# Kernel tuning notes

Hardware: AMD Instinct MI355X
Metric: run time of the kernel (lower is better)

The kernel has to match this reference:

```python
import jax, jax.numpy as jnp
import numpy as np

HEIGHT, WIDTH = 480, 640
IN_CHANNEL, OUT_CHANNEL, FILTER = 6, 32, 3
B, N = 8, 16384
X_COL, Y_COL, P_COL = 1, 2, 3


def setup_inputs() -> dict:
    key = jax.random.key(0)
    k1, k2, k3, k4 = jax.random.split(key, 4)
    xytp = jax.random.uniform(k1, (B, N, 4), dtype=jnp.float32)
    features = jax.random.normal(k2, (B, N, IN_CHANNEL), dtype=jnp.float32)
    fan_in = FILTER * FILTER * (IN_CHANNEL + 2)
    W = jax.random.normal(k3, (FILTER, FILTER, IN_CHANNEL + 2, OUT_CHANNEL), dtype=jnp.float32) / jnp.sqrt(jnp.float32(fan_in))
    bias = jax.random.normal(k4, (OUT_CHANNEL,), dtype=jnp.float32) * 0.05
    return {"xytp": xytp, "features": features, "W": W, "bias": bias}


def reference(xytp, features, W, bias):
    Bc, Nc = xytp.shape[:2]
    # polarity channels: [pos, neg] concatenated with extra features -> Cin = in_channel + 2
    p = xytp[..., P_COL:P_COL + 1]
    feat = jnp.concatenate([p, 1.0 - p, features], axis=-1)  # [B, N, Cin]
    # event2image: round normalized coords to integer pixel grid (values in [0, H] / [0, W])
    yy = jnp.round(xytp[..., Y_COL] * HEIGHT).astype(jnp.int32)  # [B, N]
    xx = jnp.round(xytp[..., X_COL] * WIDTH).astype(jnp.int32)   # [B, N]
    H1, W1 = HEIGHT + 1, WIDTH + 1
    Cin = feat.shape[-1]
    bidx = jnp.broadcast_to(jnp.arange(Bc)[:, None], (Bc, Nc))
    # scn.InputLayer(mode=3): sum features at duplicate coordinates -> dense scatter-add
    grid = jnp.zeros((Bc, H1, W1, Cin), feat.dtype).at[bidx, yy, xx].add(feat)
    # SubmanifoldConvolution: inactive sites hold zero features, so a dense SAME conv
    # computes the identical gather+GEMM+scatter result at every active site.
    out_grid = jax.lax.conv_general_dilated(
        grid, W, window_strides=(1, 1), padding='SAME',
        dimension_numbers=('NHWC', 'HWIO', 'NHWC')) + bias
    # scn.OutputLayer: each input event reads the feature at its (b, y, x) site
    return out_grid[bidx, yy, xx]  # [B, N, out_channel]
```

## Files before the change

### kernel.cpp

```cpp
#include <hip/hip_runtime.h>
#include <hip/hip_bf16.h>

#define HEIGHT 480
#define WIDTH  640
#define IN_CH  6
#define CIN    8
#define COUT   32
#define BATCH  8
#define NPTS   16384
#define NPTOT  (BATCH * NPTS)
#define GH 483
#define GW 643
#define NCELLS ((size_t)BATCH * GH * GW)
#define NW64   38824

typedef float vfloat4 __attribute__((ext_vector_type(4)));
typedef float f32x2   __attribute__((ext_vector_type(2)));

__device__ __forceinline__ size_t cell_idx(int b, int gy, int gx) {
    return ((size_t)b * GH + gy) * GW + gx;
}

__device__ __forceinline__ void point_cell(const float4 q, int point,
                                           int& b, int& gy, int& gx) {
    gy = (int)rintf(q.z * (float)HEIGHT) + 1;
    gx = (int)rintf(q.y * (float)WIDTH) + 1;
    b  = point >> 14;
}

__global__ void zero_masks_kernel(uint4* __restrict__ m4, int n4) {
    int i = blockIdx.x * blockDim.x + threadIdx.x;
    if (i < n4) m4[i] = make_uint4(0u, 0u, 0u, 0u);
}

__global__ void count_kernel(const float4* __restrict__ xytp,
                             unsigned long long* __restrict__ occ,
                             unsigned long long* __restrict__ multi,
                             float* __restrict__ grid) {
    int point = blockIdx.x * blockDim.x + threadIdx.x;
    if (point >= NPTOT) return;
    float4 q = xytp[point];
    int b, gy, gx;
    point_cell(q, point, b, gy, gx);
    size_t ci = cell_idx(b, gy, gx);
    size_t word = ci >> 6;
    unsigned long long bit = 1ull << (ci & 63);
    unsigned long long old = atomicOr(&occ[word], bit);
    if (old & bit) {
        atomicOr(&multi[word], bit);
        float* cell = grid + (ci << 3);
        const float4 z = make_float4(0.f, 0.f, 0.f, 0.f);
        *(float4*)(cell)     = z;
        *(float4*)(cell + 4) = z;
    }
}

__global__ void write_kernel(const float4* __restrict__ xytp,
                             const float*  __restrict__ feats,
                             const unsigned long long* __restrict__ multi,
                             float* __restrict__ grid) {
    int point = blockIdx.x * blockDim.x + threadIdx.x;
    if (point >= NPTOT) return;
    float4 q = xytp[point];
    int b, gy, gx;
    point_cell(q, point, b, gy, gx);
    size_t ci = cell_idx(b, gy, gx);

    const float* f = feats + (size_t)point * IN_CH;
    float v0 = q.w, v1 = 1.0f - q.w;
    float f0 = f[0], f1 = f[1], f2 = f[2], f3 = f[3], f4 = f[4], f5 = f[5];

    float* cell = grid + (ci << 3);
    if (!((multi[ci >> 6] >> (ci & 63)) & 1ull)) {
        vfloat4 a = {v0, v1, f0, f1};
        vfloat4 d = {f2, f3, f4, f5};
        __builtin_nontemporal_store(a, (vfloat4*)cell);
        __builtin_nontemporal_store(d, (vfloat4*)(cell + 4));
    } else {
        unsafeAtomicAdd(cell + 0, v0);
        unsafeAtomicAdd(cell + 1, v1);
        unsafeAtomicAdd(cell + 2, f0);
        unsafeAtomicAdd(cell + 3, f1);
        unsafeAtomicAdd(cell + 4, f2);
        unsafeAtomicAdd(cell + 5, f3);
        unsafeAtomicAdd(cell + 6, f4);
        unsafeAtomicAdd(cell + 7, f5);
    }
}

__global__ void __launch_bounds__(256)
conv_gather_kernel(const float4* __restrict__ xytp,
                   const float*  __restrict__ grid,
                   const unsigned long long* __restrict__ occ,
                   const float*  __restrict__ W,
                   const float*  __restrict__ bias,
                   float* __restrict__ out) {
    int point = blockIdx.x * blockDim.x + threadIdx.x;
    if (point >= NPTOT) return;
    float4 q = xytp[point];
    int b, gy, gx;
    point_cell(q, point, b, gy, gx);
    size_t center  = cell_idx(b, gy, gx);
    size_t base_ci = center - GW - 1;

    unsigned int occ9 = 0;
#pragma unroll
    for (int ky = 0; ky < 3; ++ky) {
        size_t ci_row = base_ci + (size_t)ky * GW;
        size_t w  = ci_row >> 6;
        int    sh = (int)(ci_row & 63);
        unsigned long long v = occ[w] >> sh;
        if (sh >= 62) v |= occ[w + 1] << (64 - sh);
        occ9 |= ((unsigned int)v & 7u) << (ky * 3);
    }

    float4 g0[9], g1[9];
#pragma unroll
    for (int k = 0; k < 9; ++k) {
        if (occ9 & (1u << k)) {
            size_t ci = base_ci + (size_t)(k / 3) * GW + (k % 3);
            const float* cell = grid + (ci << 3);
            g0[k] = *(const float4*)(cell);
            g1[k] = *(const float4*)(cell + 4);
        }
    }

    const f32x2* bias2 = (const f32x2*)bias;
    f32x2 acc[16];
#pragma unroll
    for (int c = 0; c < 16; ++c) acc[c] = bias2[c];

#pragma unroll
    for (int k = 0; k < 9; ++k) {
        if (occ9 & (1u << k)) {
            float4 a = g0[k], d = g1[k];
            float gv[CIN] = {a.x, a.y, a.z, a.w, d.x, d.y, d.z, d.w};
            const float* wp = W + k * CIN * COUT;
#pragma unroll
            for (int ci2 = 0; ci2 < CIN; ++ci2) {
                const f32x2* w2 = (const f32x2*)(wp + ci2 * COUT);
                f32x2 gg = {gv[ci2], gv[ci2]};
#pragma unroll
                for (int c = 0; c < 16; ++c) {
                    acc[c] = __builtin_elementwise_fma(gg, w2[c], acc[c]);
                }
            }
        }
    }

    float* o = out + (size_t)point * COUT;
#pragma unroll
    for (int c = 0; c < 8; ++c) {
        *(float4*)(o + c * 4) = make_float4(acc[2 * c].x, acc[2 * c].y,
                                            acc[2 * c + 1].x, acc[2 * c + 1].y);
    }
}

extern "C" void kernel_launch(void* const* d_in, const int* in_sizes, int n_in,
                              void* d_out, int out_size, void* d_ws, size_t ws_size,
                              hipStream_t stream) {
    const float4* xytp  = (const float4*)d_in[0];
    const float*  feats = (const float*)d_in[1];
    const float*  W     = (const float*)d_in[2];
    const float*  bias  = (const float*)d_in[3];
    float* out = (float*)d_out;

    float* grid = (float*)d_ws;
    const size_t grid_bytes = NCELLS * CIN * sizeof(float);
    unsigned long long* occ   = (unsigned long long*)((char*)d_ws + grid_bytes);
    unsigned long long* multi = occ + NW64;
    (void)ws_size;

    const int blk = 256;
    const int nblk_pts = (NPTOT + blk - 1) / blk;

    const int n4 = (2 * NW64 * 8) / 16;
    zero_masks_kernel<<<(n4 + blk - 1) / blk, blk, 0, stream>>>((uint4*)occ, n4);

    count_kernel<<<nblk_pts, blk, 0, stream>>>(xytp, occ, multi, grid);

    write_kernel<<<nblk_pts, blk, 0, stream>>>(xytp, feats, multi, grid);

    conv_gather_kernel<<<nblk_pts, blk, 0, stream>>>(xytp, grid, occ, W, bias, out);
}
```

Before: 41.79 us.

## Merge count and write passes; defer duplicate-site accumulation to overflow list

Replaces the separate count and write kernels with one scatter kernel. The first point to claim a cell (via atomicOr on the occupancy bitmap) writes its features directly, and later duplicates append their cell index and values to an overflow list. A small fix kernel then atomically adds the overflow entries into the grid. This drops one full pass over the points and the separate multi-bitmap, at the cost of a global atomic counter and a serialized dependency on the first writer's plain store completing before the fix kernel's atomic adds.

Result: slower. 56.12 us (+34.3%).

```diff
diff --git a/kernel.cpp b/kernel.cpp
--- a/kernel.cpp
+++ b/kernel.cpp
@@ -14,8 +14,7 @@
 #define NCELLS ((size_t)BATCH * GH * GW)
 #define NW64   38824
 
-typedef float vfloat4 __attribute__((ext_vector_type(4)));
-typedef float f32x2   __attribute__((ext_vector_type(2)));
+typedef float f32x2 __attribute__((ext_vector_type(2)));
 
 __device__ __forceinline__ size_t cell_idx(int b, int gy, int gx) {
     return ((size_t)b * GH + gy) * GW + gx;
@@ -33,32 +32,13 @@
     if (i < n4) m4[i] = make_uint4(0u, 0u, 0u, 0u);
 }
 
-__global__ void count_kernel(const float4* __restrict__ xytp,
-                             unsigned long long* __restrict__ occ,
-                             unsigned long long* __restrict__ multi,
-                             float* __restrict__ grid) {
-    int point = blockIdx.x * blockDim.x + threadIdx.x;
-    if (point >= NPTOT) return;
-    float4 q = xytp[point];
-    int b, gy, gx;
-    point_cell(q, point, b, gy, gx);
-    size_t ci = cell_idx(b, gy, gx);
-    size_t word = ci >> 6;
-    unsigned long long bit = 1ull << (ci & 63);
-    unsigned long long old = atomicOr(&occ[word], bit);
-    if (old & bit) {
-        atomicOr(&multi[word], bit);
-        float* cell = grid + (ci << 3);
-        const float4 z = make_float4(0.f, 0.f, 0.f, 0.f);
-        *(float4*)(cell)     = z;
-        *(float4*)(cell + 4) = z;
-    }
-}
-
-__global__ void write_kernel(const float4* __restrict__ xytp,
-                             const float*  __restrict__ feats,
-                             const unsigned long long* __restrict__ multi,
-                             float* __restrict__ grid) {
+__global__ void scatter_kernel(const float4* __restrict__ xytp,
+                               const float*  __restrict__ feats,
+                               unsigned long long* __restrict__ occ,
+                               unsigned int* __restrict__ n_over,
+                               unsigned int* __restrict__ over_idx,
+                               float4* __restrict__ over_val,
+                               float* __restrict__ grid) {
     int point = blockIdx.x * blockDim.x + threadIdx.x;
     if (point >= NPTOT) return;
     float4 q = xytp[point];
@@ -70,21 +50,39 @@
     float v0 = q.w, v1 = 1.0f - q.w;
     float f0 = f[0], f1 = f[1], f2 = f[2], f3 = f[3], f4 = f[4], f5 = f[5];
 
-    float* cell = grid + (ci << 3);
-    if (!((multi[ci >> 6] >> (ci & 63)) & 1ull)) {
-        vfloat4 a = {v0, v1, f0, f1};
-        vfloat4 d = {f2, f3, f4, f5};
-        __builtin_nontemporal_store(a, (vfloat4*)cell);
-        __builtin_nontemporal_store(d, (vfloat4*)(cell + 4));
+    unsigned long long bit = 1ull << (ci & 63);
+    unsigned long long old = atomicOr(&occ[ci >> 6], bit);
+    if (!(old & bit)) {
+        float* cell = grid + (ci << 3);
+        *(float4*)(cell)     = make_float4(v0, v1, f0, f1);
+        *(float4*)(cell + 4) = make_float4(f2, f3, f4, f5);
     } else {
-        unsafeAtomicAdd(cell + 0, v0);
-        unsafeAtomicAdd(cell + 1, v1);
-        unsafeAtomicAdd(cell + 2, f0);
-        unsafeAtomicAdd(cell + 3, f1);
-        unsafeAtomicAdd(cell + 4, f2);
-        unsafeAtomicAdd(cell + 5, f3);
-        unsafeAtomicAdd(cell + 6, f4);
-        unsafeAtomicAdd(cell + 7, f5);
+        unsigned int slot = atomicAdd(n_over, 1u);
+        over_idx[slot] = (unsigned int)ci;
+        over_val[2 * slot]     = make_float4(v0, v1, f0, f1);
+        over_val[2 * slot + 1] = make_float4(f2, f3, f4, f5);
+    }
+}
+
+__global__ void fix_kernel(const unsigned int* __restrict__ n_over,
+                           const unsigned int* __restrict__ over_idx,
+                           const float4* __restrict__ over_val,
+                           float* __restrict__ grid) {
+    unsigned int n = *n_over;
+    unsigned int stride = gridDim.x * blockDim.x;
+    for (unsigned int i = blockIdx.x * blockDim.x + threadIdx.x; i < n; i += stride) {
+        size_t ci = over_idx[i];
+        float4 a = over_val[2 * i];
+        float4 d = over_val[2 * i + 1];
+        float* cell = grid + (ci << 3);
+        unsafeAtomicAdd(cell + 0, a.x);
+        unsafeAtomicAdd(cell + 1, a.y);
+        unsafeAtomicAdd(cell + 2, a.z);
+        unsafeAtomicAdd(cell + 3, a.w);
+        unsafeAtomicAdd(cell + 4, d.x);
+        unsafeAtomicAdd(cell + 5, d.y);
+        unsafeAtomicAdd(cell + 6, d.z);
+        unsafeAtomicAdd(cell + 7, d.w);
     }
 }
 
@@ -167,19 +165,23 @@
 
     float* grid = (float*)d_ws;
     const size_t grid_bytes = NCELLS * CIN * sizeof(float);
-    unsigned long long* occ   = (unsigned long long*)((char*)d_ws + grid_bytes);
-    unsigned long long* multi = occ + NW64;
+    char* p = (char*)d_ws + grid_bytes;
+    unsigned int*       n_over   = (unsigned int*)p;
+    unsigned long long* occ      = (unsigned long long*)(p + 16);
+    unsigned int*       over_idx = (unsigned int*)(p + 16 + (size_t)NW64 * 8);
+    float4*             over_val = (float4*)(p + 16 + (size_t)NW64 * 8 + (size_t)NPTOT * 4);
     (void)ws_size;
 
     const int blk = 256;
     const int nblk_pts = (NPTOT + blk - 1) / blk;
 
-    const int n4 = (2 * NW64 * 8) / 16;
-    zero_masks_kernel<<<(n4 + blk - 1) / blk, blk, 0, stream>>>((uint4*)occ, n4);
+    const int n4 = (int)((16 + (size_t)NW64 * 8) / 16);
+    zero_masks_kernel<<<(n4 + blk - 1) / blk, blk, 0, stream>>>((uint4*)p, n4);
 
-    count_kernel<<<nblk_pts, blk, 0, stream>>>(xytp, occ, multi, grid);
+    scatter_kernel<<<nblk_pts, blk, 0, stream>>>(xytp, feats, occ, n_over,
+                                                 over_idx, over_val, grid);
 
-    write_kernel<<<nblk_pts, blk, 0, stream>>>(xytp, feats, multi, grid);
+    fix_kernel<<<128, blk, 0, stream>>>(n_over, over_idx, over_val, grid);
 
     conv_gather_kernel<<<nblk_pts, blk, 0, stream>>>(xytp, grid, occ, W, bias, out);
 }
```
